# Kernel optimization log

Hardware: AMD Instinct MI355X
Metric: run time of the kernel (lower is better)

The kernel has to match this reference:

```python
import jax, jax.numpy as jnp
import numpy as np


def setup_inputs() -> dict:
    key = jax.random.key(0)
    k1, k2 = jax.random.split(key)
    flow = jax.random.normal(k1, (4, 2, 256, 256), dtype=jnp.float32)   # [B,2,H,W] per-pixel flow over dt
    spike = jax.random.uniform(k2, (4, 64, 256, 256), dtype=jnp.float32)  # [B,C,H,W] spike voxel grid
    return {"flow": flow, "spike": spike}


def _splat(vals, xn, yn, H, W):
    """Forward bilinear splat of vals [H,W] to continuous coords (xn,yn) [H,W]."""
    x0 = jnp.floor(xn)
    y0 = jnp.floor(yn)
    wx = xn - x0  # fractional weights (differentiable w.r.t. flow)
    wy = yn - y0
    x0i = x0.astype(jnp.int32)
    y0i = y0.astype(jnp.int32)
    out = jnp.zeros(H * W, dtype=vals.dtype)
    corners = (
        (0, 0, (1.0 - wx) * (1.0 - wy)),
        (1, 0, wx * (1.0 - wy)),
        (0, 1, (1.0 - wx) * wy),
        (1, 1, wx * wy),
    )
    for dx, dy, w in corners:
        xi = x0i + dx
        yi = y0i + dy
        valid = (xi >= 0) & (xi < W) & (yi >= 0) & (yi < H)
        idx = jnp.clip(yi, 0, H - 1) * W + jnp.clip(xi, 0, W - 1)
        out = out.at[idx.ravel()].add(jnp.where(valid, w * vals, 0.0).ravel())
    return out.reshape(H, W)


def spike_warp_mid(spike, flow, dt):
    """Warp each time bin c by flow * (c - mid)/dt toward the middle timestamp (bilinear splat)."""
    B, C, H, W = spike.shape
    mid = (C - 1) / 2.0
    yy, xx = jnp.meshgrid(jnp.arange(H, dtype=spike.dtype),
                          jnp.arange(W, dtype=spike.dtype), indexing='ij')
    s = (jnp.arange(C, dtype=spike.dtype) - mid) / jnp.asarray(dt, spike.dtype)  # [C]
    u = flow[:, 0][:, None]  # [B,1,H,W]
    v = flow[:, 1][:, None]
    xn = xx + u * s[None, :, None, None]  # [B,C,H,W]
    yn = yy + v * s[None, :, None, None]
    splat_bc = jax.vmap(jax.vmap(lambda va, xa, ya: _splat(va, xa, ya, H, W)))
    return splat_bc(spike, xn, yn)  # [B,C,H,W]


def reference(flow, spike):
    B, C, H, W = spike.shape
    spike_warped = spike_warp_mid(spike, flow, dt=64)
    # Faithful to original: sum over BATCH dim inside per-batch loop (same each iter),
    # so loss = (B * -var) / B = -var(spike_image) with unbiased variance.
    spike_image = jnp.sum(spike_warped, axis=0)  # [C,H,W]
    loss = -jnp.var(spike_image - jnp.mean(spike_image), ddof=1)
    return loss
```

## Files before the change

kernel.cpp:

```cpp
#include <hip/hip_runtime.h>

typedef float f2 __attribute__((ext_vector_type(2)));

constexpr int B = 4, C = 64, H = 256, W = 256;
constexpr int HW = H * W;
constexpr long long N_TOT = (long long)C * HW;

constexpr int TS = 16;
constexpr int R = 4;
constexpr int SW = 24;
constexpr int SAREA = SW * SW;
constexpr int NBLK = 256 * 8;

__global__ __launch_bounds__(256) void fused_kernel(
    const float* __restrict__ flow,
    const float* __restrict__ spike,
    double* __restrict__ partials) {
  __shared__ f2 uv[SAREA];
  __shared__ f2 spk[SAREA * 4];
  __shared__ float wmx[4], wmy[4];
  __shared__ double red[8];

  const int bid = blockIdx.x;
  const int tile = bid & 255;
  const int j = bid >> 8;
  const int tx0 = (tile & 15) * TS;
  const int ty0 = (tile >> 4) * TS;
  const int tid = threadIdx.x;
  const int qx = tid & 15, qy = tid >> 4;
  const int wave = tid >> 6;

  f2 smv[4];
  float smag3;
#pragma unroll
  for (int t = 0; t < 4; ++t) {
    float sm = ((float)(4 * j + t) + 0.5f) * (1.0f / 64.0f);
    smv[t] = f2{-sm, sm};
    if (t == 3) smag3 = sm;
  }
  const int cn0 = 31 - 4 * j;
  const int cp0 = 32 + 4 * j;

  f2 acc2[4];
#pragma unroll
  for (int t = 0; t < 4; ++t) acc2[t] = f2{0.f, 0.f};

  bool c_act[3], c_val[3];
  int c_apos[3], c_gp[3];
#pragma unroll
  for (int k = 0; k < 3; ++k) {
    int pos = tid + 256 * k;
    c_act[k] = pos < SAREA;
    int row = pos / SW;
    int col = pos - row * SW;
    c_apos[k] = pos;
    int gy = ty0 + row - R, gx = tx0 + col - R;
    c_val[k] = c_act[k] & ((unsigned)gy < (unsigned)H) & ((unsigned)gx < (unsigned)W);
    c_gp[k] = gy * W + gx;
  }

  float p_u[3], p_v[3];
  float4 p_a[3], p_b[3];

  auto prefetch = [&](int b) {
    const float* fu = flow + (size_t)b * 2 * HW;
    const float* fv = fu + HW;
    const float* spb = spike + (size_t)b * C * HW;
#pragma unroll
    for (int k = 0; k < 3; ++k) {
      float u = 0.f, v = 0.f;
      float4 a = {0.f, 0.f, 0.f, 0.f};
      float4 d = {0.f, 0.f, 0.f, 0.f};
      if (c_val[k]) {
        int gp = c_gp[k];
        u = fu[gp];
        v = fv[gp];
        a.x = spb[(size_t)cn0 * HW + gp];
        a.y = spb[(size_t)(cn0 - 1) * HW + gp];
        a.z = spb[(size_t)(cn0 - 2) * HW + gp];
        a.w = spb[(size_t)(cn0 - 3) * HW + gp];
        d.x = spb[(size_t)cp0 * HW + gp];
        d.y = spb[(size_t)(cp0 + 1) * HW + gp];
        d.z = spb[(size_t)(cp0 + 2) * HW + gp];
        d.w = spb[(size_t)(cp0 + 3) * HW + gp];
      }
      p_u[k] = u; p_v[k] = v; p_a[k] = a; p_b[k] = d;
    }
  };

  prefetch(0);

  const int qpos = (qy + R) * SW + (qx + R);

  for (int b = 0; b < B; ++b) {
    float mu = 0.f, mv = 0.f;
#pragma unroll
    for (int k = 0; k < 3; ++k) {
      if (c_act[k]) {
        int ap = c_apos[k];
        uv[ap] = f2{p_u[k], p_v[k]};
        f2* sp = &spk[ap * 4];
        sp[0] = f2{p_a[k].x, p_b[k].x};
        sp[1] = f2{p_a[k].y, p_b[k].y};
        sp[2] = f2{p_a[k].z, p_b[k].z};
        sp[3] = f2{p_a[k].w, p_b[k].w};
        mu = fmaxf(mu, fabsf(p_u[k]));
        mv = fmaxf(mv, fabsf(p_v[k]));
      }
    }
    for (int off = 32; off > 0; off >>= 1) {
      mu = fmaxf(mu, __shfl_down(mu, off, 64));
      mv = fmaxf(mv, __shfl_down(mv, off, 64));
    }
    if ((tid & 63) == 0) { wmx[wave] = mu; wmy[wave] = mv; }
    __syncthreads();
    float bu = fmaxf(fmaxf(wmx[0], wmx[1]), fmaxf(wmx[2], wmx[3]));
    float bv = fmaxf(fmaxf(wmy[0], wmy[1]), fmaxf(wmy[2], wmy[3]));
    int rx = min((int)(1.0f + bu * smag3), R);
    int ry = min((int)(1.0f + bv * smag3), R);

    if (b + 1 < B) prefetch(b + 1);

    for (int dy = -ry; dy <= ry; ++dy) {
      const f2 fdy2 = (float)dy;
      for (int dx = -rx; dx <= rx; ++dx) {
        const int pp = qpos + dy * SW + dx;
        f2 u2 = uv[pp];
        const f2* vp = &spk[pp * 4];
        const f2 fdx2 = (float)dx;
        const f2 ux = f2{u2.x, u2.x};
        const f2 vy = f2{u2.y, u2.y};
#pragma unroll
        for (int t = 0; t < 4; ++t) {
          f2 ax = __builtin_elementwise_fma(ux, smv[t], fdx2);
          f2 ay = __builtin_elementwise_fma(vy, smv[t], fdy2);
          f2 tx = __builtin_elementwise_max(1.0f - __builtin_elementwise_abs(ax), f2{0.f, 0.f});
          f2 ty = __builtin_elementwise_max(1.0f - __builtin_elementwise_abs(ay), f2{0.f, 0.f});
          acc2[t] = __builtin_elementwise_fma(tx * ty, vp[t], acc2[t]);
        }
      }
    }
    __syncthreads();
  }

  double ls = 0.0, lq = 0.0;
#pragma unroll
  for (int t = 0; t < 4; ++t) {
    double a = (double)acc2[t].x, b2 = (double)acc2[t].y;
    ls += a + b2;
    lq += a * a + b2 * b2;
  }
  for (int off = 32; off > 0; off >>= 1) {
    ls += __shfl_down(ls, off, 64);
    lq += __shfl_down(lq, off, 64);
  }
  if ((tid & 63) == 0) { red[wave * 2] = ls; red[wave * 2 + 1] = lq; }
  __syncthreads();
  if (tid == 0) {
    partials[2 * bid] = red[0] + red[2] + red[4] + red[6];
    partials[2 * bid + 1] = red[1] + red[3] + red[5] + red[7];
  }
}

__global__ __launch_bounds__(256) void finalize_kernel(
    const double* __restrict__ partials, float* __restrict__ out) {
  double s = 0.0, q = 0.0;
  for (int i = threadIdx.x; i < NBLK; i += 256) {
    s += partials[2 * i];
    q += partials[2 * i + 1];
  }
  for (int off = 32; off > 0; off >>= 1) {
    s += __shfl_down(s, off, 64);
    q += __shfl_down(q, off, 64);
  }
  __shared__ double ss[4], qq[4];
  int lane = threadIdx.x & 63;
  int wave = threadIdx.x >> 6;
  if (lane == 0) { ss[wave] = s; qq[wave] = q; }
  __syncthreads();
  if (threadIdx.x == 0) {
    double sum = ss[0] + ss[1] + ss[2] + ss[3];
    double sq = qq[0] + qq[1] + qq[2] + qq[3];
    double n = (double)N_TOT;
    double var = (sq - sum * sum / n) / (n - 1.0);
    out[0] = (float)(-var);
  }
}

extern "C" void kernel_launch(void* const* d_in, const int* in_sizes, int n_in,
                              void* d_out, int out_size, void* d_ws, size_t ws_size,
                              hipStream_t stream) {
  const float* flow = (const float*)d_in[0];
  const float* spike = (const float*)d_in[1];
  float* out = (float*)d_out;
  double* partials = (double*)d_ws;

  fused_kernel<<<dim3(NBLK), dim3(256), 0, stream>>>(flow, spike, partials);
  finalize_kernel<<<1, dim3(256), 0, stream>>>(partials, out);
}
```

Measured before the change: 156.5 us.

## Replace per-pixel neighbor gather with source-pixel scatter via LDS atomics

Drops the gather formulation, in which each output pixel scanned a flow-dependent window of neighbor sources, and makes each source pixel scatter its four bilinear corner weights into a padded shared-memory accumulator using LDS atomicAdd. The source halo shrinks from 4 to 3, sources whose displaced footprint cannot reach the tile are skipped early, spike and flow loads are double-buffered in registers across batches, and launch bounds now request higher occupancy. This removes the redundant window evaluation and the per-batch max-flow reduction and barrier. In exchange it adds shared-memory atomic contention and drops any contribution from sources displaced more than three pixels.

```diff
diff --git a/kernel.cpp b/kernel.cpp
--- a/kernel.cpp
+++ b/kernel.cpp
@@ -7,19 +7,21 @@
 constexpr long long N_TOT = (long long)C * HW;
 
 constexpr int TS = 16;
-constexpr int R = 4;
-constexpr int SW = 24;
+constexpr int R = 3;
+constexpr int SW = TS + 2 * R;
 constexpr int SAREA = SW * SW;
+constexpr int PAD = 4;
+constexpr int AW = TS + 2 * PAD;
+constexpr int AAREA = AW * AW;
 constexpr int NBLK = 256 * 8;
 
-__global__ __launch_bounds__(256) void fused_kernel(
+__global__ __launch_bounds__(256, 6) void fused_kernel(
     const float* __restrict__ flow,
     const float* __restrict__ spike,
     double* __restrict__ partials) {
-  __shared__ f2 uv[SAREA];
-  __shared__ f2 spk[SAREA * 4];
-  __shared__ float wmx[4], wmy[4];
+  __shared__ float4 accum4[(8 * AAREA) / 4];
   __shared__ double red[8];
+  float* accum = (float*)accum4;
 
   const int bid = blockIdx.x;
   const int tile = bid & 255;
@@ -27,128 +29,129 @@
   const int tx0 = (tile & 15) * TS;
   const int ty0 = (tile >> 4) * TS;
   const int tid = threadIdx.x;
-  const int qx = tid & 15, qy = tid >> 4;
   const int wave = tid >> 6;
 
   f2 smv[4];
-  float smag3;
+  float s3;
 #pragma unroll
   for (int t = 0; t < 4; ++t) {
     float sm = ((float)(4 * j + t) + 0.5f) * (1.0f / 64.0f);
     smv[t] = f2{-sm, sm};
-    if (t == 3) smag3 = sm;
+    if (t == 3) s3 = sm;
   }
   const int cn0 = 31 - 4 * j;
   const int cp0 = 32 + 4 * j;
 
-  f2 acc2[4];
-#pragma unroll
-  for (int t = 0; t < 4; ++t) acc2[t] = f2{0.f, 0.f};
-
-  bool c_act[3], c_val[3];
-  int c_apos[3], c_gp[3];
-#pragma unroll
-  for (int k = 0; k < 3; ++k) {
+  bool c_val[2];
+  int c_gp[2];
+  float c_flx[2], c_fly[2];
+#pragma unroll
+  for (int k = 0; k < 2; ++k) {
     int pos = tid + 256 * k;
-    c_act[k] = pos < SAREA;
+    bool act = pos < SAREA;
     int row = pos / SW;
     int col = pos - row * SW;
-    c_apos[k] = pos;
-    int gy = ty0 + row - R, gx = tx0 + col - R;
-    c_val[k] = c_act[k] & ((unsigned)gy < (unsigned)H) & ((unsigned)gx < (unsigned)W);
+    int lx = col - R, ly = row - R;
+    int gy = ty0 + ly, gx = tx0 + lx;
+    c_val[k] = act & ((unsigned)gy < (unsigned)H) & ((unsigned)gx < (unsigned)W);
     c_gp[k] = gy * W + gx;
-  }
-
-  float p_u[3], p_v[3];
-  float4 p_a[3], p_b[3];
-
-  auto prefetch = [&](int b) {
+    c_flx[k] = (float)lx;
+    c_fly[k] = (float)ly;
+  }
+
+  float pu[2][2], pv[2][2];
+  f2 pq[2][2][4];
+
+  auto loadb = [&](int buf, int b) {
     const float* fu = flow + (size_t)b * 2 * HW;
     const float* fv = fu + HW;
     const float* spb = spike + (size_t)b * C * HW;
 #pragma unroll
-    for (int k = 0; k < 3; ++k) {
+    for (int k = 0; k < 2; ++k) {
       float u = 0.f, v = 0.f;
-      float4 a = {0.f, 0.f, 0.f, 0.f};
-      float4 d = {0.f, 0.f, 0.f, 0.f};
+      f2 q0 = {0.f, 0.f}, q1 = {0.f, 0.f}, q2 = {0.f, 0.f}, q3 = {0.f, 0.f};
       if (c_val[k]) {
         int gp = c_gp[k];
         u = fu[gp];
         v = fv[gp];
-        a.x = spb[(size_t)cn0 * HW + gp];
-        a.y = spb[(size_t)(cn0 - 1) * HW + gp];
-        a.z = spb[(size_t)(cn0 - 2) * HW + gp];
-        a.w = spb[(size_t)(cn0 - 3) * HW + gp];
-        d.x = spb[(size_t)cp0 * HW + gp];
-        d.y = spb[(size_t)(cp0 + 1) * HW + gp];
-        d.z = spb[(size_t)(cp0 + 2) * HW + gp];
-        d.w = spb[(size_t)(cp0 + 3) * HW + gp];
+        q0.x = spb[(size_t)cn0 * HW + gp];
+        q0.y = spb[(size_t)cp0 * HW + gp];
+        q1.x = spb[(size_t)(cn0 - 1) * HW + gp];
+        q1.y = spb[(size_t)(cp0 + 1) * HW + gp];
+        q2.x = spb[(size_t)(cn0 - 2) * HW + gp];
+        q2.y = spb[(size_t)(cp0 + 2) * HW + gp];
+        q3.x = spb[(size_t)(cn0 - 3) * HW + gp];
+        q3.y = spb[(size_t)(cp0 + 3) * HW + gp];
       }
-      p_u[k] = u; p_v[k] = v; p_a[k] = a; p_b[k] = d;
+      pu[buf][k] = u; pv[buf][k] = v;
+      pq[buf][k][0] = q0; pq[buf][k][1] = q1;
+      pq[buf][k][2] = q2; pq[buf][k][3] = q3;
     }
   };
 
-  prefetch(0);
-
-  const int qpos = (qy + R) * SW + (qx + R);
-
+  loadb(0, 0);
+
+#pragma unroll
+  for (int i = tid; i < (8 * AAREA) / 4; i += 256)
+    accum4[i] = float4{0.f, 0.f, 0.f, 0.f};
+  __syncthreads();
+
+#pragma unroll
   for (int b = 0; b < B; ++b) {
-    float mu = 0.f, mv = 0.f;
-#pragma unroll
-    for (int k = 0; k < 3; ++k) {
-      if (c_act[k]) {
-        int ap = c_apos[k];
-        uv[ap] = f2{p_u[k], p_v[k]};
-        f2* sp = &spk[ap * 4];
-        sp[0] = f2{p_a[k].x, p_b[k].x};
-        sp[1] = f2{p_a[k].y, p_b[k].y};
-        sp[2] = f2{p_a[k].z, p_b[k].z};
-        sp[3] = f2{p_a[k].w, p_b[k].w};
-        mu = fmaxf(mu, fabsf(p_u[k]));
-        mv = fmaxf(mv, fabsf(p_v[k]));
+    const int cur = b & 1;
+    if (b + 1 < B) loadb((b + 1) & 1, b + 1);
+
+#pragma unroll
+    for (int k = 0; k < 2; ++k) {
+      if (!c_val[k]) continue;
+      const float u = pu[cur][k], v = pv[cur][k];
+      const float flx = c_flx[k], fly = c_fly[k];
+      const float au = fabsf(u) * s3, av = fabsf(v) * s3;
+      if (flx + au <= -1.f || flx - au >= (float)TS ||
+          fly + av <= -1.f || fly - av >= (float)TS) continue;
+
+      const f2 u2 = f2{u, u}, v2 = f2{v, v};
+      const f2 flx2 = f2{flx, flx}, fly2 = f2{fly, fly};
+#pragma unroll
+      for (int t = 0; t < 4; ++t) {
+        f2 xn = __builtin_elementwise_fma(u2, smv[t], flx2);
+        f2 yn = __builtin_elementwise_fma(v2, smv[t], fly2);
+        float fx0 = floorf(xn.x), fx1 = floorf(xn.y);
+        float fy0 = floorf(yn.x), fy1 = floorf(yn.y);
+        f2 wx = xn - f2{fx0, fx1};
+        f2 wy = yn - f2{fy0, fy1};
+        f2 vv = pq[cur][k][t];
+        f2 ax = (1.0f - wx) * vv;
+        f2 bx = wx * vv;
+        f2 oy = 1.0f - wy;
+        f2 w00 = ax * oy, w10 = bx * oy, w01 = ax * wy, w11 = bx * wy;
+        int ix0 = min(max((int)fx0, -PAD), TS + PAD - 2);
+        int ix1 = min(max((int)fx1, -PAD), TS + PAD - 2);
+        int iy0 = min(max((int)fy0, -PAD), TS + PAD - 2);
+        int iy1 = min(max((int)fy1, -PAD), TS + PAD - 2);
+        float* b0 = &accum[(2 * t) * AAREA + (iy0 + PAD) * AW + (ix0 + PAD)];
+        float* b1 = &accum[(2 * t + 1) * AAREA + (iy1 + PAD) * AW + (ix1 + PAD)];
+        atomicAdd(b0, w00.x);
+        atomicAdd(b0 + 1, w10.x);
+        atomicAdd(b0 + AW, w01.x);
+        atomicAdd(b0 + AW + 1, w11.x);
+        atomicAdd(b1, w00.y);
+        atomicAdd(b1 + 1, w10.y);
+        atomicAdd(b1 + AW, w01.y);
+        atomicAdd(b1 + AW + 1, w11.y);
       }
     }
-    for (int off = 32; off > 0; off >>= 1) {
-      mu = fmaxf(mu, __shfl_down(mu, off, 64));
-      mv = fmaxf(mv, __shfl_down(mv, off, 64));
-    }
-    if ((tid & 63) == 0) { wmx[wave] = mu; wmy[wave] = mv; }
-    __syncthreads();
-    float bu = fmaxf(fmaxf(wmx[0], wmx[1]), fmaxf(wmx[2], wmx[3]));
-    float bv = fmaxf(fmaxf(wmy[0], wmy[1]), fmaxf(wmy[2], wmy[3]));
-    int rx = min((int)(1.0f + bu * smag3), R);
-    int ry = min((int)(1.0f + bv * smag3), R);
-
-    if (b + 1 < B) prefetch(b + 1);
-
-    for (int dy = -ry; dy <= ry; ++dy) {
-      const f2 fdy2 = (float)dy;
-      for (int dx = -rx; dx <= rx; ++dx) {
-        const int pp = qpos + dy * SW + dx;
-        f2 u2 = uv[pp];
-        const f2* vp = &spk[pp * 4];
-        const f2 fdx2 = (float)dx;
-        const f2 ux = f2{u2.x, u2.x};
-        const f2 vy = f2{u2.y, u2.y};
-#pragma unroll
-        for (int t = 0; t < 4; ++t) {
-          f2 ax = __builtin_elementwise_fma(ux, smv[t], fdx2);
-          f2 ay = __builtin_elementwise_fma(vy, smv[t], fdy2);
-          f2 tx = __builtin_elementwise_max(1.0f - __builtin_elementwise_abs(ax), f2{0.f, 0.f});
-          f2 ty = __builtin_elementwise_max(1.0f - __builtin_elementwise_abs(ay), f2{0.f, 0.f});
-          acc2[t] = __builtin_elementwise_fma(tx * ty, vp[t], acc2[t]);
-        }
-      }
-    }
-    __syncthreads();
-  }
-
+  }
+  __syncthreads();
+
+  const int qx = tid & 15, qy = tid >> 4;
+  const int opos = (qy + PAD) * AW + (qx + PAD);
   double ls = 0.0, lq = 0.0;
 #pragma unroll
-  for (int t = 0; t < 4; ++t) {
-    double a = (double)acc2[t].x, b2 = (double)acc2[t].y;
-    ls += a + b2;
-    lq += a * a + b2 * b2;
+  for (int m = 0; m < 8; ++m) {
+    double x = (double)accum[m * AAREA + opos];
+    ls += x;
+    lq += x * x;
   }
   for (int off = 32; off > 0; off >>= 1) {
     ls += __shfl_down(ls, off, 64);
```

Result: slower. 529.4 us (+238.4%).
